# Optimization experiments

Measured on AMD Instinct MI355X. Metric: run time of the kernel, lower is better.

The kernel has to match this reference:

```python
import jax, jax.numpy as jnp
import numpy as np

H = 50  # hidden size (hardcoded in the torch module)

def lstm_cell(h, c, xt, Wih, Whh, bih, bhh):
    # xt: [B, D]; gates packed PyTorch-style: i, f, g, o each of size H
    gates = xt @ Wih.T + h @ Whh.T + bih + bhh  # [B, 4H]
    i, f, g, o = jnp.split(gates, 4, axis=-1)
    i = jax.nn.sigmoid(i)
    f = jax.nn.sigmoid(f)
    g = jnp.tanh(g)
    o = jax.nn.sigmoid(o)
    c_new = f * c + i * g
    h_new = o * jnp.tanh(c_new)
    return h_new, c_new

def lstm_last_hidden(x, Wih, Whh, bih, bhh):
    # x: [B, T, D] -> final hidden state h_T: [B, H] (zero init state)
    B = x.shape[0]
    h0 = jnp.zeros((B, H), dtype=x.dtype)
    c0 = jnp.zeros((B, H), dtype=x.dtype)
    def step(carry, xt):
        h, c = carry
        h, c = lstm_cell(h, c, xt, Wih, Whh, bih, bhh)
        return (h, c), None
    (hT, _), _ = jax.lax.scan(step, (h0, c0), jnp.swapaxes(x, 0, 1))
    return hT

def setup_inputs() -> dict:
    key = jax.random.key(0)
    ks = jax.random.split(key, 11)
    s = 1.0 / np.sqrt(H)  # PyTorch LSTM/Linear init scale
    u = lambda k, shape: jax.random.uniform(k, shape, jnp.float32, -s, s)
    return {
        'x': jax.random.normal(ks[0], (2048, 1024, 1), jnp.float32),
        'lstm1_Wih': u(ks[1], (4 * H, 1)),
        'lstm1_Whh': u(ks[2], (4 * H, H)),
        'lstm1_bih': u(ks[3], (4 * H,)),
        'lstm1_bhh': u(ks[4], (4 * H,)),
        'lstm2_Wih': u(ks[5], (4 * H, H)),
        'lstm2_Whh': u(ks[6], (4 * H, H)),
        'lstm2_bih': u(ks[7], (4 * H,)),
        'lstm2_bhh': u(ks[8], (4 * H,)),
        'fc_W': u(ks[9], (1, H)),
        'fc_b': u(ks[10], (1,)),
    }

def reference(x, lstm1_Wih, lstm1_Whh, lstm1_bih, lstm1_bhh,
              lstm2_Wih, lstm2_Whh, lstm2_bih, lstm2_bhh, fc_W, fc_b):
    # lstm1 over full sequence; only the last timestep output is used downstream
    h1 = lstm_last_hidden(x, lstm1_Wih, lstm1_Whh, lstm1_bih, lstm1_bhh)  # [B, H]
    # lstm2 sees a length-1 sequence starting from zero state -> one cell step
    B = x.shape[0]
    z = jnp.zeros((B, H), dtype=x.dtype)
    h2, _ = lstm_cell(z, z, h1, lstm2_Wih, lstm2_Whh, lstm2_bih, lstm2_bhh)  # [B, H]
    return h2 @ fc_W.T + fc_b  # [B, 1]
```

## Files before the change

kernel.cpp:

```cpp
#include <hip/hip_runtime.h>

#define HH 50
#define TT 1024
#define BT 8
#define NB (2048 / BT)
#define XSTF 1028
#define HST 72

typedef _Float16 half8 __attribute__((ext_vector_type(8)));
typedef float f32x4 __attribute__((ext_vector_type(4)));

union H8 { half8 v; _Float16 h[8]; unsigned short u[8]; unsigned int i[4]; };

__device__ __forceinline__ float rcp_f(float x) { return __builtin_amdgcn_rcpf(x); }

#if __has_builtin(__builtin_amdgcn_exp2f)
__device__ __forceinline__ float exp2_f(float x) { return __builtin_amdgcn_exp2f(x); }
#else
__device__ __forceinline__ float exp2_f(float x) { return __expf(0.6931471805599453f * x); }
#endif

#define L2E   1.4426950408889634f
#define L2E2  2.8853900817779268f

__device__ __forceinline__ float sigm_n(float a) {
    return rcp_f(1.0f + exp2_f(a));
}
__device__ __forceinline__ float tanh_p(float a) {
    return __builtin_fmaf(-2.0f, rcp_f(1.0f + exp2_f(a)), 1.0f);
}
__device__ __forceinline__ unsigned short f2h(float f) {
    return __builtin_bit_cast(unsigned short, (_Float16)f);
}

__global__ __launch_bounds__(256) void lstm_mfma_kernel(
    const float* __restrict__ x,
    const float* __restrict__ wih1, const float* __restrict__ whh1,
    const float* __restrict__ bih1, const float* __restrict__ bhh1,
    const float* __restrict__ wih2,
    const float* __restrict__ bih2, const float* __restrict__ bhh2,
    const float* __restrict__ fcw,  const float* __restrict__ fcb,
    float* __restrict__ out)
{
    __shared__ float xs[BT * XSTF];
    __shared__ __align__(16) unsigned short hb[2][16 * HST];
    __shared__ float h2s[BT * 52];

    const int tid  = threadIdx.x;
    const int wv   = tid >> 6;
    const int js   = wv;
    const int lane = tid & 63;
    const int l16  = lane & 15;
    const int quad = lane >> 4;
    const int j    = js * 16 + l16;
    const bool jv  = (j < HH);
    const bool q2  = (quad == 2);
    const int b0   = blockIdx.x * BT;
    const int  bm0   = ((quad & 1) << 2) + ((quad >> 1) << 1);

    H8 bw[4][2];
    #pragma unroll
    for (int t4 = 0; t4 < 4; ++t4) {
        const float sc = (t4 == 2) ? L2E2 : -L2E;
        const int row = t4 * HH + j;
        #pragma unroll
        for (int kk = 0; kk < 2; ++kk)
            #pragma unroll
            for (int e = 0; e < 8; ++e) {
                const int k = kk * 32 + quad * 8 + e;
                const float v = (jv && k < HH) ? whh1[row * HH + k] * sc : 0.0f;
                bw[t4][kk].h[e] = (_Float16)v;
            }
        if (q2) {
            const float bsc = jv ? (bih1[row] + bhh1[row]) * sc : 0.0f;
            const _Float16 bhi = (_Float16)bsc;
            bw[t4][1].h[2] = (_Float16)(jv ? wih1[row] * sc : 0.0f);
            bw[t4][1].h[3] = bhi;
            bw[t4][1].h[4] = (_Float16)(bsc - (float)bhi);
        }
    }

    for (int i = tid; i < 2 * 16 * HST; i += 256) {
        const int col = i % HST;
        ((unsigned short*)hb)[i] = (col == 51 || col == 52) ? 0x3c00 : 0;
    }

    for (int i = tid; i < BT * (TT / 4); i += 256) {
        const int r = i >> 8, c4 = i & 255;
        const float4 q = ((const float4*)x)[((b0 + r) * TT) / 4 + c4];
        *(float4*)&xs[r * XSTF + c4 * 4] = q;
    }
    if (tid < BT * 4) xs[(tid >> 2) * XSTF + 1024 + (tid & 3)] = 0.0f;
    __syncthreads();

    const bool xw = (wv == 0) && (lane < BT);
    if (xw) hb[0][lane * HST + 50] = f2h(xs[lane * XSTF]);
    __syncthreads();

    float c0 = 0.f, c1 = 0.f;
    const f32x4 kZ = {0.f, 0.f, 0.f, 0.f};

    auto cell = [&](float ai, float af, float ag, float ao, float& cc) -> unsigned short {
        const float Ei = exp2_f(ai), Ef = exp2_f(af), Eg = exp2_f(ag), Eo = exp2_f(ao);
        const float pf  = 1.0f + Ef;
        const float P   = (1.0f + Ei) * (1.0f + Eg);
        const float den = pf * P;
        const float num = __builtin_fmaf(cc, P, (Eg - 1.0f) * pf);
        cc = num * rcp_f(den);
        const float ac = fminf(cc * L2E2, 80.0f);
        const float Ec = exp2_f(ac);
        const float h  = (Ec - 1.0f) * rcp_f((1.0f + Eo) * (1.0f + Ec));
        return f2h(h);
    };

#define REDIST(G, P0, P1)                                                      \
    {                                                                          \
        float a_ = acc[G][0], b_ = acc[G][1];                                  \
        float c_ = acc[G][2], d_ = acc[G][3];                                  \
        asm("v_permlane32_swap_b32 %0, %1" : "+v"(a_), "+v"(c_));              \
        asm("v_permlane32_swap_b32 %0, %1" : "+v"(b_), "+v"(d_));              \
        P0 = a_;                                                               \
        P1 = b_;                                                               \
    }

#define STEP(T, CUR, NXT)                                                      \
    {                                                                          \
        H8 a0, a1;                                                             \
        a0.v = *(const half8*)&(CUR)[l16 * HST + quad * 8];                    \
        a1.v = *(const half8*)&(CUR)[l16 * HST + 32 + quad * 8];               \
        float xnext = 0.0f;                                                    \
        if (xw) xnext = xs[lane * XSTF + (T) + 1];                             \
        f32x4 acc[4];                                                          \
        _Pragma("unroll")                                                      \
        for (int t4 = 0; t4 < 4; ++t4) {                                       \
            acc[t4] = __builtin_amdgcn_mfma_f32_16x16x32_f16(a0.v, bw[t4][0].v, kZ, 0, 0, 0);       \
            acc[t4] = __builtin_amdgcn_mfma_f32_16x16x32_f16(a1.v, bw[t4][1].v, acc[t4], 0, 0, 0);  \
        }                                                                      \
        float pi0, pi1, pf0, pf1, pg0, pg1, po0, po1;                          \
        REDIST(0, pi0, pi1) REDIST(1, pf0, pf1)                                \
        REDIST(2, pg0, pg1) REDIST(3, po0, po1)                                \
        const unsigned short h0 = cell(pi0, pf0, pg0, po0, c0);                \
        const unsigned short h1 = cell(pi1, pf1, pg1, po1, c1);                \
        if (jv) {        \
            (NXT)[bm0 * HST + j]       = h0;                                   \
            (NXT)[(bm0 + 1) * HST + j] = h1;                                   \
        }                                                                      \
        if (xw) (NXT)[lane * HST + 50] = f2h(xnext);                           \
        __syncthreads();                                                       \
    }

    for (int t = 0; t < TT; t += 2) {
        STEP(t,     hb[0], hb[1]);
        STEP(t + 1, hb[1], hb[0]);
    }
#undef STEP
#undef REDIST
    unsigned short* cur = hb[0];

    {
        H8 bw2[4][2];
        float b2[4];
        #pragma unroll
        for (int t4 = 0; t4 < 4; ++t4) {
            const float sc = (t4 == 2) ? L2E2 : -L2E;
            const int row = t4 * HH + j;
            #pragma unroll
            for (int kk = 0; kk < 2; ++kk)
                #pragma unroll
                for (int e = 0; e < 8; ++e) {
                    const int k = kk * 32 + quad * 8 + e;
                    const float v = (jv && k < HH) ? wih2[row * HH + k] * sc : 0.0f;
                    bw2[t4][kk].h[e] = (_Float16)v;
                }
            b2[t4] = jv ? (bih2[row] + bhh2[row]) * sc : 0.0f;
        }
        H8 a0, a1;
        a0.v = *(const half8*)&cur[l16 * HST + quad * 8];
        a1.v = *(const half8*)&cur[l16 * HST + 32 + quad * 8];
        f32x4 acc2[4];
        #pragma unroll
        for (int t4 = 0; t4 < 4; ++t4) {
            const f32x4 cb = {b2[t4], b2[t4], b2[t4], b2[t4]};
            acc2[t4] = __builtin_amdgcn_mfma_f32_16x16x32_f16(a0.v, bw2[t4][0].v, cb, 0, 0, 0);
            acc2[t4] = __builtin_amdgcn_mfma_f32_16x16x32_f16(a1.v, bw2[t4][1].v, acc2[t4], 0, 0, 0);
        }
        #pragma unroll
        for (int r = 0; r < 4; ++r) {
            const int b = quad * 4 + r;
            const float ig = sigm_n(acc2[0][r]);
            const float gg = tanh_p(acc2[2][r]);
            const float og = sigm_n(acc2[3][r]);
            const float cc = ig * gg;
            const float h2 = og * tanh_p(cc * L2E2);
            if (b < BT && jv) h2s[b * 52 + j] = h2;
        }
    }
    __syncthreads();

    if (tid < BT * 16) {
        const int b = tid >> 4, l = tid & 15;
        float p = 0.f;
        for (int jj = l; jj < HH; jj += 16)
            p = __builtin_fmaf(h2s[b * 52 + jj], fcw[jj], p);
        #pragma unroll
        for (int off = 8; off > 0; off >>= 1) p += __shfl_xor(p, off, 16);
        if (l == 0) out[b0 + b] = p + fcb[0];
    }
}

extern "C" void kernel_launch(void* const* d_in, const int* in_sizes, int n_in,
                              void* d_out, int out_size, void* d_ws, size_t ws_size,
                              hipStream_t stream) {
    lstm_mfma_kernel<<<NB, 256, 0, stream>>>(
        (const float*)d_in[0],
        (const float*)d_in[1], (const float*)d_in[2],
        (const float*)d_in[3], (const float*)d_in[4],
        (const float*)d_in[5],
        (const float*)d_in[7], (const float*)d_in[8],
        (const float*)d_in[9], (const float*)d_in[10],
        (float*)d_out);
}
```

Measured before the change: 432.3 us.

## XOR-swizzle hidden-state LDS layout, store x as fp16 transposed, remove branchy writes

```diff
diff --git a/kernel.cpp b/kernel.cpp
--- a/kernel.cpp
+++ b/kernel.cpp
@@ -4,8 +4,8 @@
 #define TT 1024
 #define BT 8
 #define NB (2048 / BT)
-#define XSTF 1028
 #define HST 72
+#define HBUF (16 * HST)
 
 typedef _Float16 half8 __attribute__((ext_vector_type(8)));
 typedef float f32x4 __attribute__((ext_vector_type(4)));
@@ -32,6 +32,7 @@
 __device__ __forceinline__ unsigned short f2h(float f) {
     return __builtin_bit_cast(unsigned short, (_Float16)f);
 }
+
 
 __global__ __launch_bounds__(256) void lstm_mfma_kernel(
     const float* __restrict__ x,
@@ -42,8 +43,8 @@
     const float* __restrict__ fcw,  const float* __restrict__ fcb,
     float* __restrict__ out)
 {
-    __shared__ float xs[BT * XSTF];
-    __shared__ __align__(16) unsigned short hb[2][16 * HST];
+    __shared__ __align__(16) unsigned short hb[2][HBUF];
+    __shared__ unsigned short xh[(TT + 2) * BT];
     __shared__ float h2s[BT * 52];
 
     const int tid  = threadIdx.x;
@@ -56,7 +57,7 @@
     const bool jv  = (j < HH);
     const bool q2  = (quad == 2);
     const int b0   = blockIdx.x * BT;
-    const int  bm0   = ((quad & 1) << 2) + ((quad >> 1) << 1);
+    const int bm0 = ((quad & 1) << 2) + ((quad >> 1) << 1);
 
     H8 bw[4][2];
     #pragma unroll
@@ -80,22 +81,44 @@
         }
     }
 
-    for (int i = tid; i < 2 * 16 * HST; i += 256) {
-        const int col = i % HST;
-        ((unsigned short*)hb)[i] = (col == 51 || col == 52) ? 0x3c00 : 0;
+    for (int i = tid; i < 2 * HBUF; i += 256) {
+        const int colL = i % HST;
+        const int row  = (i / HST) & 15;
+        unsigned short v = 0;
+        if (colL < 64) {
+            const int colU = (((colL >> 3) ^ (row & 7)) << 3) | (colL & 7);
+            if (colU == 51 || colU == 52) v = 0x3c00;
+        }
+        ((unsigned short*)hb)[i] = v;
     }
 
     for (int i = tid; i < BT * (TT / 4); i += 256) {
         const int r = i >> 8, c4 = i & 255;
         const float4 q = ((const float4*)x)[((b0 + r) * TT) / 4 + c4];
-        *(float4*)&xs[r * XSTF + c4 * 4] = q;
-    }
-    if (tid < BT * 4) xs[(tid >> 2) * XSTF + 1024 + (tid & 3)] = 0.0f;
+        const int t0 = c4 * 4;
+        xh[(t0 + 0) * BT + r] = f2h(q.x);
+        xh[(t0 + 1) * BT + r] = f2h(q.y);
+        xh[(t0 + 2) * BT + r] = f2h(q.z);
+        xh[(t0 + 3) * BT + r] = f2h(q.w);
+    }
+    if (tid < 2 * BT) xh[TT * BT + tid] = 0;
     __syncthreads();
 
-    const bool xw = (wv == 0) && (lane < BT);
-    if (xw) hb[0][lane * HST + 50] = f2h(xs[lane * XSTF]);
+    if (wv == 0 && lane < BT)
+        hb[0][lane * HST + ((6 ^ (lane & 7)) << 3) + 2] = xh[lane];
     __syncthreads();
+
+    const int swq  = l16 & 7;
+    const int ra0o = l16 * HST + ((quad ^ swq) << 3);
+    const int ra1o = l16 * HST + (((4 + quad) ^ swq) << 3);
+    const int r0  = jv ? bm0 : (8 + (bm0 & 7));
+    const int r1  = r0 + 1;
+    const int jb  = j >> 3, jo = j & 7;
+    const int wa0 = r0 * HST + ((jb ^ (r0 & 7)) << 3) + jo;
+    const int wa1 = r1 * HST + ((jb ^ (r1 & 7)) << 3) + jo;
+    const int xrow = (wv == 0 && lane < BT) ? lane : (8 + (lane & 7));
+    const int wx   = xrow * HST + ((6 ^ (xrow & 7)) << 3) + 2;
+    const int xsub = lane & 7;
 
     float c0 = 0.f, c1 = 0.f;
     const f32x4 kZ = {0.f, 0.f, 0.f, 0.f};
@@ -123,13 +146,12 @@
         P1 = b_;                                                               \
     }
 
-#define STEP(T, CUR, NXT)                                                      \
+#define STEP(T, CB, NBUF)                                                      \
     {                                                                          \
         H8 a0, a1;                                                             \
-        a0.v = *(const half8*)&(CUR)[l16 * HST + quad * 8];                    \
-        a1.v = *(const half8*)&(CUR)[l16 * HST + 32 + quad * 8];               \
-        float xnext = 0.0f;                                                    \
-        if (xw) xnext = xs[lane * XSTF + (T) + 1];                             \
+        a0.v = *(const half8*)&hb[CB][ra0o];                                   \
+        a1.v = *(const half8*)&hb[CB][ra1o];                                   \
+        const unsigned short xn = xh[((T) + 1) * BT + xsub];    \
         f32x4 acc[4];                                                          \
         _Pragma("unroll")                                                      \
         for (int t4 = 0; t4 < 4; ++t4) {                                       \
@@ -141,21 +163,18 @@
         REDIST(2, pg0, pg1) REDIST(3, po0, po1)                                \
         const unsigned short h0 = cell(pi0, pf0, pg0, po0, c0);                \
         const unsigned short h1 = cell(pi1, pf1, pg1, po1, c1);                \
-        if (jv) {        \
-            (NXT)[bm0 * HST + j]       = h0;                                   \
-            (NXT)[(bm0 + 1) * HST + j] = h1;                                   \
-        }                                                                      \
-        if (xw) (NXT)[lane * HST + 50] = f2h(xnext);                           \
+        hb[NBUF][wa0] = h0;                                                    \
+        hb[NBUF][wa1] = h1;                                                    \
+        hb[NBUF][wx]  = xn;            \
         __syncthreads();                                                       \
     }
 
     for (int t = 0; t < TT; t += 2) {
-        STEP(t,     hb[0], hb[1]);
-        STEP(t + 1, hb[1], hb[0]);
+        STEP(t,     0, 1);
+        STEP(t + 1, 1, 0);
     }
 #undef STEP
 #undef REDIST
-    unsigned short* cur = hb[0];
 
     {
         H8 bw2[4][2];
@@ -175,8 +194,8 @@
             b2[t4] = jv ? (bih2[row] + bhh2[row]) * sc : 0.0f;
         }
         H8 a0, a1;
-        a0.v = *(const half8*)&cur[l16 * HST + quad * 8];
-        a1.v = *(const half8*)&cur[l16 * HST + 32 + quad * 8];
+        a0.v = *(const half8*)&hb[0][ra0o];
+        a1.v = *(const half8*)&hb[0][ra1o];
         f32x4 acc2[4];
         #pragma unroll
         for (int t4 = 0; t4 < 4; ++t4) {
```

After: 451.3 us. +4.4%, slower.
